# Kernel optimization log

Measured on AMD Instinct MI355X. Metric: run time of the kernel, lower is better.

The kernel has to match this reference:

```python
import jax, jax.numpy as jnp
import numpy as np


def rotate_half(x):
    x1, x2 = jnp.split(x, 2, axis=-1)
    return jnp.concatenate([-x2, x1], axis=-1)


def setup_inputs() -> dict:
    key = jax.random.key(0)
    ks = jax.random.split(key, 12)
    B, T, D, H, HD, MS = 1, 128, 4096, 32, 128, 8192
    s = 0.02  # weight init scale
    return {
        "x": jax.random.normal(ks[0], (B, T, D), jnp.float32),
        "wq_w": jax.random.normal(ks[1], (D, D), jnp.float32) * s,
        "wq_b": jax.random.normal(ks[2], (D,), jnp.float32) * s,
        "wk_w": jax.random.normal(ks[3], (D, D), jnp.float32) * s,
        "wk_b": jax.random.normal(ks[4], (D,), jnp.float32) * s,
        "wv_w": jax.random.normal(ks[5], (D, D), jnp.float32) * s,
        "wv_b": jax.random.normal(ks[6], (D,), jnp.float32) * s,
        "wo_w": jax.random.normal(ks[7], (D, D), jnp.float32) * s,
        "wo_b": jax.random.normal(ks[8], (D,), jnp.float32) * s,
        "k_cache": jax.random.normal(ks[9], (MS, H, HD), jnp.float32),
        "v_cache": jax.random.normal(ks[10], (MS, H, HD), jnp.float32),
        "pos": 4096,        # RoPE position scalar (as in source: single pos)
        "cache_pos": 4096,  # static write offset into the KV cache
    }


def reference(x, wq_w, wq_b, wk_w, wk_b, wv_w, wv_b, wo_w, wo_b,
              k_cache, v_cache, pos, cache_pos):
    B, T, D = x.shape
    H, HD = k_cache.shape[1], k_cache.shape[2]

    q = (x @ wq_w.T + wq_b).reshape(B, T, H, HD)
    k = (x @ wk_w.T + wk_b).reshape(B, T, H, HD)
    v = (x @ wv_w.T + wv_b).reshape(B, T, H, HD)

    # KV-cache append (B == 1, matching source's squeeze(0))
    k_cache = jax.lax.dynamic_update_slice(k_cache, k[0], (cache_pos, 0, 0))
    v_cache = jax.lax.dynamic_update_slice(v_cache, v[0], (cache_pos, 0, 0))
    S = cache_pos + T

    # inline RoPE at scalar position `pos` on q and the full live cache
    inv_freq = 1.0 / (10000.0 ** (jnp.arange(0, HD, 2, dtype=jnp.float32) / HD))
    ang = pos * inv_freq                      # [HD/2]
    sin = jnp.concatenate([jnp.sin(ang)] * 2) # [HD]
    cos = jnp.concatenate([jnp.cos(ang)] * 2) # [HD]

    kc = k_cache[:S][None]                    # [1, S, H, HD]
    vc = v_cache[:S][None]                    # [1, S, H, HD]
    q_rot = q * cos + rotate_half(q) * sin
    k_rot = kc * cos + rotate_half(kc) * sin

    scale = 1.0 / np.sqrt(HD).astype(np.float32)
    scores = jnp.einsum('bthd,bshd->bhts', q_rot, k_rot) * scale  # [B,H,T,S]
    attn = jax.nn.softmax(scores, axis=-1)
    out = jnp.einsum('bhts,bshd->bthd', attn, vc).reshape(B, T, D)
    return out @ wo_w.T + wo_b
```

## Files before the change

kernel.cpp:

```cpp
#include <hip/hip_runtime.h>

#define TQ     128
#define DIM    4096
#define NHEAD  32
#define HDIM   128
#define CPOS   4096
#define NCHUNK 8

typedef __attribute__((ext_vector_type(8))) short short8;
typedef __attribute__((ext_vector_type(4))) float f32x4;

__device__ __forceinline__ unsigned short f2bf(float f) {
    union { float f; unsigned int u; } v; v.f = f;
    unsigned int r = v.u + 0x7FFFu + ((v.u >> 16) & 1u);
    return (unsigned short)(r >> 16);
}

__global__ __launch_bounds__(256) void cvt_x_kernel(const float* __restrict__ x,
                                                    unsigned short* __restrict__ xbf) {
    int i = blockIdx.x * 256 + threadIdx.x;
    float4 v = ((const float4*)x)[i];
    union { unsigned short u[4]; uint2 w; } o;
    o.u[0] = f2bf(v.x); o.u[1] = f2bf(v.y); o.u[2] = f2bf(v.z); o.u[3] = f2bf(v.w);
    ((uint2*)xbf)[i] = o.w;
}

__global__ __launch_bounds__(256, 2) void qkv_gemm_kernel(
    const unsigned short* __restrict__ xbf,
    const float* __restrict__ wq, const float* __restrict__ wk, const float* __restrict__ wv,
    const float* __restrict__ bq, const float* __restrict__ bk, const float* __restrict__ bv,
    unsigned short* __restrict__ qbf, unsigned short* __restrict__ kbf,
    unsigned short* __restrict__ vbf)
{
    __shared__ unsigned short As[128 * 40];
    __shared__ unsigned short Bs[48 * 40];
    const int tid = threadIdx.x;
    const int w = tid >> 6, lane = tid & 63;
    const int q = lane >> 4, j = lane & 15;
    const int ncol0 = blockIdx.x * 48;

    f32x4 acc[2][3];
#pragma unroll
    for (int mi = 0; mi < 2; ++mi)
#pragma unroll
        for (int ni = 0; ni < 3; ++ni) acc[mi][ni] = (f32x4){0.f, 0.f, 0.f, 0.f};

    for (int it = 0; it < 128; ++it) {
        const int k0 = it * 32;
#pragma unroll
        for (int g = tid; g < 512; g += 256) {
            int row = g >> 2, col8 = (g & 3) * 8;
            uint4 d = *(const uint4*)(xbf + (size_t)row * DIM + k0 + col8);
            *(uint4*)(As + row * 40 + col8) = d;
        }
#pragma unroll
        for (int f = tid; f < 384; f += 256) {
            int row = f >> 3, col4 = (f & 7) * 4;
            int n = ncol0 + row;
            const float* wp = (n < 4096) ? wq : ((n < 8192) ? wk : wv);
            float4 d = *(const float4*)(wp + (size_t)(n & 4095) * DIM + k0 + col4);
            union { unsigned short u[4]; uint2 v; } o;
            o.u[0] = f2bf(d.x); o.u[1] = f2bf(d.y); o.u[2] = f2bf(d.z); o.u[3] = f2bf(d.w);
            *(uint2*)(Bs + row * 40 + col4) = o.v;
        }
        __syncthreads();
        short8 af[2], bfr[3];
#pragma unroll
        for (int mi = 0; mi < 2; ++mi)
            af[mi] = *(const short8*)(As + (w * 32 + mi * 16 + j) * 40 + q * 8);
#pragma unroll
        for (int ni = 0; ni < 3; ++ni)
            bfr[ni] = *(const short8*)(Bs + (ni * 16 + j) * 40 + q * 8);
#pragma unroll
        for (int mi = 0; mi < 2; ++mi)
#pragma unroll
            for (int ni = 0; ni < 3; ++ni)
                acc[mi][ni] = __builtin_amdgcn_mfma_f32_16x16x32_bf16(af[mi], bfr[ni], acc[mi][ni], 0, 0, 0);
        __syncthreads();
    }
#pragma unroll
    for (int ni = 0; ni < 3; ++ni) {
        int col = ncol0 + ni * 16 + j;
        int mat = col >> 12, nn = col & 4095;
        const float* bp = (mat == 0) ? bq : ((mat == 1) ? bk : bv);
        unsigned short* op = (mat == 0) ? qbf : ((mat == 1) ? kbf : vbf);
        float bias = bp[nn];
#pragma unroll
        for (int mi = 0; mi < 2; ++mi)
#pragma unroll
            for (int r = 0; r < 4; ++r) {
                int t = w * 32 + mi * 16 + q * 4 + r;
                op[(size_t)t * DIM + nn] = f2bf(acc[mi][ni][r] + bias);
            }
    }
}

__global__ __launch_bounds__(256, 2) void attn_kernel(
    const unsigned short* __restrict__ qbf, const unsigned short* __restrict__ kbf,
    const unsigned short* __restrict__ vbf,
    const float* __restrict__ kcache, const float* __restrict__ vcache,
    float* __restrict__ opart, float* __restrict__ ml)
{
    __shared__ unsigned short Ks[64 * 136];
    __shared__ unsigned short Vt[128 * 68];
    __shared__ unsigned short Ps[128 * 72];
    const int tid = threadIdx.x;
    const int w = tid >> 6, lane = tid & 63;
    const int q = lane >> 4, j = lane & 15;
    const int c = blockIdx.x, h = blockIdx.y;
    const int ntiles = (c == NCHUNK - 1) ? 10 : 8;
    const int s_base = c * 512;
    const float scale = 0.088388347648318447f;

    short8 qf[2][4];
#pragma unroll
    for (int mi = 0; mi < 2; ++mi) {
        int t = w * 32 + mi * 16 + j;
#pragma unroll
        for (int ks = 0; ks < 4; ++ks)
            qf[mi][ks] = *(const short8*)(qbf + (size_t)t * DIM + h * HDIM + ks * 32 + q * 8);
    }

    f32x4 oacc[2][8];
    float m_st[2][4], l_st[2][4];
#pragma unroll
    for (int mi = 0; mi < 2; ++mi) {
#pragma unroll
        for (int nh = 0; nh < 8; ++nh) oacc[mi][nh] = (f32x4){0.f, 0.f, 0.f, 0.f};
#pragma unroll
        for (int r = 0; r < 4; ++r) { m_st[mi][r] = -1e30f; l_st[mi][r] = 0.f; }
    }

    for (int tile = 0; tile < ntiles; ++tile) {
        const int s0 = s_base + tile * 64;
        const bool from_new = (s0 >= CPOS);
        if (!from_new) {
#pragma unroll
            for (int i = 0; i < 8; ++i) {
                int f = tid + i * 256;
                int row = f >> 5, col4 = (f & 31) * 4;
                float4 d = *(const float4*)(kcache + (size_t)(s0 + row) * DIM + h * HDIM + col4);
                union { unsigned short u[4]; uint2 v; } o;
                o.u[0] = f2bf(d.x); o.u[1] = f2bf(d.y); o.u[2] = f2bf(d.z); o.u[3] = f2bf(d.w);
                *(uint2*)(Ks + row * 136 + col4) = o.v;
            }
        } else {
            int sn = s0 - CPOS;
#pragma unroll
            for (int i = 0; i < 4; ++i) {
                int g = tid + i * 256;
                int row = g >> 4, col8 = (g & 15) * 8;
                uint4 d = *(const uint4*)(kbf + (size_t)(sn + row) * DIM + h * HDIM + col8);
                *(uint4*)(Ks + row * 136 + col8) = d;
            }
        }
        if (!from_new) {
#pragma unroll
            for (int i = 0; i < 2; ++i) {
                int ch = tid + i * 256;
                int s4 = ch >> 5, col4 = (ch & 31) * 4;
                const float* src = vcache + (size_t)(s0 + s4 * 4) * DIM + h * HDIM + col4;
                float4 r0 = *(const float4*)(src);
                float4 r1 = *(const float4*)(src + DIM);
                float4 r2 = *(const float4*)(src + 2 * DIM);
                float4 r3 = *(const float4*)(src + 3 * DIM);
#pragma unroll
                for (int i2 = 0; i2 < 4; ++i2) {
                    union { unsigned short u[4]; uint2 v; } o;
                    o.u[0] = f2bf((&r0.x)[i2]); o.u[1] = f2bf((&r1.x)[i2]);
                    o.u[2] = f2bf((&r2.x)[i2]); o.u[3] = f2bf((&r3.x)[i2]);
                    *(uint2*)(Vt + (col4 + i2) * 68 + s4 * 4) = o.v;
                }
            }
        } else {
            int sn = s0 - CPOS;
#pragma unroll
            for (int i = 0; i < 2; ++i) {
                int ch = tid + i * 256;
                int s4 = ch >> 5, col4 = (ch & 31) * 4;
                const unsigned short* src = vbf + (size_t)(sn + s4 * 4) * DIM + h * HDIM + col4;
                union { uint2 v; unsigned short u[4]; } a0, a1, a2, a3;
                a0.v = *(const uint2*)(src);
                a1.v = *(const uint2*)(src + DIM);
                a2.v = *(const uint2*)(src + 2 * DIM);
                a3.v = *(const uint2*)(src + 3 * DIM);
#pragma unroll
                for (int i2 = 0; i2 < 4; ++i2) {
                    union { unsigned short u[4]; uint2 v; } o;
                    o.u[0] = a0.u[i2]; o.u[1] = a1.u[i2]; o.u[2] = a2.u[i2]; o.u[3] = a3.u[i2];
                    *(uint2*)(Vt + (col4 + i2) * 68 + s4 * 4) = o.v;
                }
            }
        }
        __syncthreads();

        f32x4 sacc[2][4];
#pragma unroll
        for (int mi = 0; mi < 2; ++mi)
#pragma unroll
            for (int ni = 0; ni < 4; ++ni) sacc[mi][ni] = (f32x4){0.f, 0.f, 0.f, 0.f};
#pragma unroll
        for (int ks = 0; ks < 4; ++ks) {
            short8 kb[4];
#pragma unroll
            for (int ni = 0; ni < 4; ++ni)
                kb[ni] = *(const short8*)(Ks + (ni * 16 + j) * 136 + ks * 32 + q * 8);
#pragma unroll
            for (int mi = 0; mi < 2; ++mi)
#pragma unroll
                for (int ni = 0; ni < 4; ++ni)
                    sacc[mi][ni] = __builtin_amdgcn_mfma_f32_16x16x32_bf16(qf[mi][ks], kb[ni], sacc[mi][ni], 0, 0, 0);
        }

#pragma unroll
        for (int mi = 0; mi < 2; ++mi) {
            float alpha[4];
#pragma unroll
            for (int r = 0; r < 4; ++r) {
                float v = sacc[mi][0][r];
#pragma unroll
                for (int ni = 1; ni < 4; ++ni) v = fmaxf(v, sacc[mi][ni][r]);
#pragma unroll
                for (int mask = 1; mask < 16; mask <<= 1)
                    v = fmaxf(v, __shfl_xor(v, mask, 64));
                float mnew = fmaxf(m_st[mi][r], v * scale);
                alpha[r] = __expf(m_st[mi][r] - mnew);
                m_st[mi][r] = mnew;
            }
#pragma unroll
            for (int ni = 0; ni < 4; ++ni)
#pragma unroll
                for (int r = 0; r < 4; ++r)
                    sacc[mi][ni][r] = __expf(sacc[mi][ni][r] * scale - m_st[mi][r]);
#pragma unroll
            for (int r = 0; r < 4; ++r) {
                float s = sacc[mi][0][r] + sacc[mi][1][r] + sacc[mi][2][r] + sacc[mi][3][r];
#pragma unroll
                for (int mask = 1; mask < 16; mask <<= 1)
                    s += __shfl_xor(s, mask, 64);
                l_st[mi][r] = l_st[mi][r] * alpha[r] + s;
            }
#pragma unroll
            for (int ni = 0; ni < 4; ++ni)
#pragma unroll
                for (int r = 0; r < 4; ++r)
                    Ps[(w * 32 + mi * 16 + q * 4 + r) * 72 + ni * 16 + j] = f2bf(sacc[mi][ni][r]);
#pragma unroll
            for (int nh = 0; nh < 8; ++nh)
#pragma unroll
                for (int r = 0; r < 4; ++r)
                    oacc[mi][nh][r] *= alpha[r];
        }

#pragma unroll
        for (int ks2 = 0; ks2 < 2; ++ks2) {
            short8 pa[2];
#pragma unroll
            for (int mi = 0; mi < 2; ++mi)
                pa[mi] = *(const short8*)(Ps + (w * 32 + mi * 16 + j) * 72 + ks2 * 32 + q * 8);
#pragma unroll
            for (int nh = 0; nh < 8; ++nh) {
                const unsigned short* p = Vt + (nh * 16 + j) * 68 + ks2 * 32 + q * 8;
                uint2 lo = *(const uint2*)p, hi = *(const uint2*)(p + 4);
                union { unsigned int w4[4]; short8 s; } u;
                u.w4[0] = lo.x; u.w4[1] = lo.y; u.w4[2] = hi.x; u.w4[3] = hi.y;
#pragma unroll
                for (int mi = 0; mi < 2; ++mi)
                    oacc[mi][nh] = __builtin_amdgcn_mfma_f32_16x16x32_bf16(pa[mi], u.s, oacc[mi][nh], 0, 0, 0);
            }
        }
        __syncthreads();
    }

    float* op = opart + ((size_t)(h * NCHUNK + c) * TQ) * HDIM;
#pragma unroll
    for (int mi = 0; mi < 2; ++mi)
#pragma unroll
        for (int nh = 0; nh < 8; ++nh)
#pragma unroll
            for (int r = 0; r < 4; ++r) {
                int t = w * 32 + mi * 16 + q * 4 + r;
                op[(size_t)t * HDIM + nh * 16 + j] = oacc[mi][nh][r];
            }
    if (j == 0) {
        float* mlp = ml + (size_t)(h * NCHUNK + c) * TQ * 2;
#pragma unroll
        for (int mi = 0; mi < 2; ++mi)
#pragma unroll
            for (int r = 0; r < 4; ++r) {
                int t = w * 32 + mi * 16 + q * 4 + r;
                mlp[t * 2] = m_st[mi][r];
                mlp[t * 2 + 1] = l_st[mi][r];
            }
    }
}

__global__ __launch_bounds__(128) void combine_kernel(const float* __restrict__ opart,
                                                      const float* __restrict__ ml,
                                                      unsigned short* __restrict__ abf) {
    int t = blockIdx.x, h = blockIdx.y, hd = threadIdx.x;
    float mv[NCHUNK], lv[NCHUNK];
    float M = -1e30f;
#pragma unroll
    for (int c = 0; c < NCHUNK; ++c) {
        mv[c] = ml[(size_t)((h * NCHUNK + c) * TQ + t) * 2];
        lv[c] = ml[(size_t)((h * NCHUNK + c) * TQ + t) * 2 + 1];
        M = fmaxf(M, mv[c]);
    }
    float L = 0.f, acc = 0.f;
#pragma unroll
    for (int c = 0; c < NCHUNK; ++c) {
        float wgt = __expf(mv[c] - M);
        L += wgt * lv[c];
        acc += wgt * opart[((size_t)(h * NCHUNK + c) * TQ + t) * HDIM + hd];
    }
    abf[(size_t)t * DIM + h * HDIM + hd] = f2bf(acc / L);
}

__global__ __launch_bounds__(256, 2) void out_gemm_kernel(
    const unsigned short* __restrict__ abf, const float* __restrict__ wo,
    const float* __restrict__ bo, float* __restrict__ out)
{
    __shared__ unsigned short As[128 * 40];
    __shared__ unsigned short Bs[32 * 40];
    const int tid = threadIdx.x;
    const int w = tid >> 6, lane = tid & 63;
    const int q = lane >> 4, j = lane & 15;
    const int ncol0 = (blockIdx.x & 127) * 32;
    const int kc = blockIdx.x >> 7;

    f32x4 acc[2][2];
#pragma unroll
    for (int mi = 0; mi < 2; ++mi)
#pragma unroll
        for (int ni = 0; ni < 2; ++ni) acc[mi][ni] = (f32x4){0.f, 0.f, 0.f, 0.f};

    for (int it = 0; it < 64; ++it) {
        const int k0 = kc * 2048 + it * 32;
#pragma unroll
        for (int g = tid; g < 512; g += 256) {
            int row = g >> 2, col8 = (g & 3) * 8;
            uint4 d = *(const uint4*)(abf + (size_t)row * DIM + k0 + col8);
            *(uint4*)(As + row * 40 + col8) = d;
        }
        {
            int row = tid >> 3, col4 = (tid & 7) * 4;
            float4 d = *(const float4*)(wo + (size_t)(ncol0 + row) * DIM + k0 + col4);
            union { unsigned short u[4]; uint2 v; } o;
            o.u[0] = f2bf(d.x); o.u[1] = f2bf(d.y); o.u[2] = f2bf(d.z); o.u[3] = f2bf(d.w);
            *(uint2*)(Bs + row * 40 + col4) = o.v;
        }
        __syncthreads();
        short8 af[2], bfr[2];
#pragma unroll
        for (int mi = 0; mi < 2; ++mi)
            af[mi] = *(const short8*)(As + (w * 32 + mi * 16 + j) * 40 + q * 8);
#pragma unroll
        for (int ni = 0; ni < 2; ++ni)
            bfr[ni] = *(const short8*)(Bs + (ni * 16 + j) * 40 + q * 8);
#pragma unroll
        for (int mi = 0; mi < 2; ++mi)
#pragma unroll
            for (int ni = 0; ni < 2; ++ni)
                acc[mi][ni] = __builtin_amdgcn_mfma_f32_16x16x32_bf16(af[mi], bfr[ni], acc[mi][ni], 0, 0, 0);
        __syncthreads();
    }
#pragma unroll
    for (int ni = 0; ni < 2; ++ni) {
        int col = ncol0 + ni * 16 + j;
        float bias = (kc == 0) ? bo[col] : 0.f;
#pragma unroll
        for (int mi = 0; mi < 2; ++mi)
#pragma unroll
            for (int r = 0; r < 4; ++r) {
                int t = w * 32 + mi * 16 + q * 4 + r;
                atomicAdd(out + (size_t)t * DIM + col, acc[mi][ni][r] + bias);
            }
    }
}

extern "C" void kernel_launch(void* const* d_in, const int* in_sizes, int n_in,
                              void* d_out, int out_size, void* d_ws, size_t ws_size,
                              hipStream_t stream) {
    const float* x      = (const float*)d_in[0];
    const float* wq     = (const float*)d_in[1];
    const float* bq     = (const float*)d_in[2];
    const float* wk     = (const float*)d_in[3];
    const float* bk     = (const float*)d_in[4];
    const float* wv     = (const float*)d_in[5];
    const float* bv     = (const float*)d_in[6];
    const float* wo     = (const float*)d_in[7];
    const float* bo     = (const float*)d_in[8];
    const float* kcache = (const float*)d_in[9];
    const float* vcache = (const float*)d_in[10];
    float* out = (float*)d_out;

    char* ws = (char*)d_ws;
    unsigned short* xbf = (unsigned short*)(ws);
    unsigned short* qbf = (unsigned short*)(ws + (1u << 20));
    unsigned short* kbf = (unsigned short*)(ws + 2u * (1u << 20));
    unsigned short* vbf = (unsigned short*)(ws + 3u * (1u << 20));
    unsigned short* abf = (unsigned short*)(ws + 4u * (1u << 20));
    float* opart = (float*)(ws + 5u * (1u << 20));
    float* mlbuf = (float*)(ws + 21u * (1u << 20));

    hipLaunchKernelGGL(cvt_x_kernel, dim3(512), dim3(256), 0, stream, x, xbf);
    hipLaunchKernelGGL(qkv_gemm_kernel, dim3(256), dim3(256), 0, stream,
                       xbf, wq, wk, wv, bq, bk, bv, qbf, kbf, vbf);
    hipLaunchKernelGGL(attn_kernel, dim3(NCHUNK, NHEAD), dim3(256), 0, stream,
                       qbf, kbf, vbf, kcache, vcache, opart, mlbuf);
    hipLaunchKernelGGL(combine_kernel, dim3(TQ, NHEAD), dim3(128), 0, stream,
                       opart, mlbuf, abf);
    hipMemsetAsync(d_out, 0, (size_t)out_size * sizeof(float), stream);
    hipLaunchKernelGGL(out_gemm_kernel, dim3(256), dim3(256), 0, stream, abf, wo, bo, out);
}
```

Baseline: 683.6 us.

## Split-K QKV and output GEMMs with reductions, more attention chunks, register prefetch

The QKV GEMM is split along K across a second grid dimension, writes fp32 partials, and a new reduce kernel adds bias and converts to bf16. The output GEMM drops atomics and memset in favour of split-K partials plus a reduce kernel. Attention uses more sequence chunks, with a dedicated chunk for the new tokens. The GEMMs now use 64-wide K tiles with register double-buffered global loads and higher launch-bounds occupancy. Together these add parallelism on a 256-CU device at the cost of extra partial-buffer traffic and two more launches.

```diff
diff --git a/kernel.cpp b/kernel.cpp
--- a/kernel.cpp
+++ b/kernel.cpp
@@ -5,7 +5,6 @@
 #define NHEAD  32
 #define HDIM   128
 #define CPOS   4096
-#define NCHUNK 8
 
 typedef __attribute__((ext_vector_type(8))) short short8;
 typedef __attribute__((ext_vector_type(4))) float f32x4;
@@ -25,19 +24,21 @@
     ((uint2*)xbf)[i] = o.w;
 }
 
-__global__ __launch_bounds__(256, 2) void qkv_gemm_kernel(
+__global__ __launch_bounds__(256, 4) void qkv_gemm_kernel(
     const unsigned short* __restrict__ xbf,
     const float* __restrict__ wq, const float* __restrict__ wk, const float* __restrict__ wv,
-    const float* __restrict__ bq, const float* __restrict__ bk, const float* __restrict__ bv,
-    unsigned short* __restrict__ qbf, unsigned short* __restrict__ kbf,
-    unsigned short* __restrict__ vbf)
+    float* __restrict__ part)
 {
-    __shared__ unsigned short As[128 * 40];
-    __shared__ unsigned short Bs[48 * 40];
+    __shared__ unsigned short As[128 * 72];
+    __shared__ unsigned short Bs[48 * 72];
     const int tid = threadIdx.x;
     const int w = tid >> 6, lane = tid & 63;
     const int q = lane >> 4, j = lane & 15;
     const int ncol0 = blockIdx.x * 48;
+    const int kc = blockIdx.y, KS = gridDim.y;
+    const int kchunk = DIM / KS;
+    const int iters = kchunk / 64;
+    const int kbase = kc * kchunk;
 
     f32x4 acc[2][3];
 #pragma unroll
@@ -45,61 +46,114 @@
 #pragma unroll
         for (int ni = 0; ni < 3; ++ni) acc[mi][ni] = (f32x4){0.f, 0.f, 0.f, 0.f};
 
-    for (int it = 0; it < 128; ++it) {
-        const int k0 = it * 32;
-#pragma unroll
-        for (int g = tid; g < 512; g += 256) {
-            int row = g >> 2, col8 = (g & 3) * 8;
-            uint4 d = *(const uint4*)(xbf + (size_t)row * DIM + k0 + col8);
-            *(uint4*)(As + row * 40 + col8) = d;
-        }
-#pragma unroll
-        for (int f = tid; f < 384; f += 256) {
-            int row = f >> 3, col4 = (f & 7) * 4;
-            int n = ncol0 + row;
+    uint4 aReg[4];
+    float4 bReg[3];
+    {
+        const int k0 = kbase;
+#pragma unroll
+        for (int i = 0; i < 4; ++i) {
+            int flat = i * 256 + tid;
+            aReg[i] = *(const uint4*)(xbf + (size_t)(flat >> 3) * DIM + k0 + (flat & 7) * 8);
+        }
+#pragma unroll
+        for (int i = 0; i < 3; ++i) {
+            int flat = i * 256 + tid;
+            int n = ncol0 + (flat >> 4);
             const float* wp = (n < 4096) ? wq : ((n < 8192) ? wk : wv);
-            float4 d = *(const float4*)(wp + (size_t)(n & 4095) * DIM + k0 + col4);
+            bReg[i] = *(const float4*)(wp + (size_t)(n & 4095) * DIM + k0 + (flat & 15) * 4);
+        }
+    }
+
+    for (int it = 0; it < iters; ++it) {
+        if (it > 0) __syncthreads();
+#pragma unroll
+        for (int i = 0; i < 4; ++i) {
+            int flat = i * 256 + tid;
+            *(uint4*)(As + (flat >> 3) * 72 + (flat & 7) * 8) = aReg[i];
+        }
+#pragma unroll
+        for (int i = 0; i < 3; ++i) {
+            int flat = i * 256 + tid;
             union { unsigned short u[4]; uint2 v; } o;
-            o.u[0] = f2bf(d.x); o.u[1] = f2bf(d.y); o.u[2] = f2bf(d.z); o.u[3] = f2bf(d.w);
-            *(uint2*)(Bs + row * 40 + col4) = o.v;
+            o.u[0] = f2bf(bReg[i].x); o.u[1] = f2bf(bReg[i].y);
+            o.u[2] = f2bf(bReg[i].z); o.u[3] = f2bf(bReg[i].w);
+            *(uint2*)(Bs + (flat >> 4) * 72 + (flat & 15) * 4) = o.v;
         }
         __syncthreads();
-        short8 af[2], bfr[3];
-#pragma unroll
-        for (int mi = 0; mi < 2; ++mi)
-            af[mi] = *(const short8*)(As + (w * 32 + mi * 16 + j) * 40 + q * 8);
-#pragma unroll
-        for (int ni = 0; ni < 3; ++ni)
-            bfr[ni] = *(const short8*)(Bs + (ni * 16 + j) * 40 + q * 8);
-#pragma unroll
-        for (int mi = 0; mi < 2; ++mi)
+        if (it + 1 < iters) {
+            const int k0 = kbase + (it + 1) * 64;
+#pragma unroll
+            for (int i = 0; i < 4; ++i) {
+                int flat = i * 256 + tid;
+                aReg[i] = *(const uint4*)(xbf + (size_t)(flat >> 3) * DIM + k0 + (flat & 7) * 8);
+            }
+#pragma unroll
+            for (int i = 0; i < 3; ++i) {
+                int flat = i * 256 + tid;
+                int n = ncol0 + (flat >> 4);
+                const float* wp = (n < 4096) ? wq : ((n < 8192) ? wk : wv);
+                bReg[i] = *(const float4*)(wp + (size_t)(n & 4095) * DIM + k0 + (flat & 15) * 4);
+            }
+        }
+#pragma unroll
+        for (int ks = 0; ks < 2; ++ks) {
+            short8 af[2], bfr[3];
+#pragma unroll
+            for (int mi = 0; mi < 2; ++mi)
+                af[mi] = *(const short8*)(As + (w * 32 + mi * 16 + j) * 72 + ks * 32 + q * 8);
 #pragma unroll
             for (int ni = 0; ni < 3; ++ni)
-                acc[mi][ni] = __builtin_amdgcn_mfma_f32_16x16x32_bf16(af[mi], bfr[ni], acc[mi][ni], 0, 0, 0);
-        __syncthreads();
-    }
+                bfr[ni] = *(const short8*)(Bs + (ni * 16 + j) * 72 + ks * 32 + q * 8);
+#pragma unroll
+            for (int mi = 0; mi < 2; ++mi)
+#pragma unroll
+                for (int ni = 0; ni < 3; ++ni)
+                    acc[mi][ni] = __builtin_amdgcn_mfma_f32_16x16x32_bf16(af[mi], bfr[ni], acc[mi][ni], 0, 0, 0);
+        }
+    }
+    float* pp = part + (size_t)kc * (TQ * 12288);
 #pragma unroll
     for (int ni = 0; ni < 3; ++ni) {
         int col = ncol0 + ni * 16 + j;
-        int mat = col >> 12, nn = col & 4095;
-        const float* bp = (mat == 0) ? bq : ((mat == 1) ? bk : bv);
-        unsigned short* op = (mat == 0) ? qbf : ((mat == 1) ? kbf : vbf);
-        float bias = bp[nn];
 #pragma unroll
         for (int mi = 0; mi < 2; ++mi)
 #pragma unroll
             for (int r = 0; r < 4; ++r) {
                 int t = w * 32 + mi * 16 + q * 4 + r;
-                op[(size_t)t * DIM + nn] = f2bf(acc[mi][ni][r] + bias);
-            }
-    }
+                pp[(size_t)t * 12288 + col] = acc[mi][ni][r];
+            }
+    }
+}
+
+__global__ __launch_bounds__(256) void qkv_reduce_kernel(
+    const float* __restrict__ part,
+    const float* __restrict__ bq, const float* __restrict__ bk, const float* __restrict__ bv,
+    unsigned short* __restrict__ qbf, unsigned short* __restrict__ kbf,
+    unsigned short* __restrict__ vbf, int KS)
+{
+    int idx4 = blockIdx.x * 256 + threadIdx.x;
+    size_t idx = (size_t)idx4 * 4;
+    int t = (int)(idx / 12288), n = (int)(idx % 12288);
+    float4 s = *(const float4*)(part + idx);
+    for (int kc = 1; kc < KS; ++kc) {
+        float4 p = *(const float4*)(part + (size_t)kc * (TQ * 12288) + idx);
+        s.x += p.x; s.y += p.y; s.z += p.z; s.w += p.w;
+    }
+    int mat = n >> 12, nn = n & 4095;
+    const float* bp = (mat == 0) ? bq : ((mat == 1) ? bk : bv);
+    unsigned short* op = (mat == 0) ? qbf : ((mat == 1) ? kbf : vbf);
+    float4 b = *(const float4*)(bp + nn);
+    union { unsigned short u[4]; uint2 v; } o;
+    o.u[0] = f2bf(s.x + b.x); o.u[1] = f2bf(s.y + b.y);
+    o.u[2] = f2bf(s.z + b.z); o.u[3] = f2bf(s.w + b.w);
+    *(uint2*)(op + (size_t)t * 4096 + nn) = o.v;
 }
 
 __global__ __launch_bounds__(256, 2) void attn_kernel(
     const unsigned short* __restrict__ qbf, const unsigned short* __restrict__ kbf,
     const unsigned short* __restrict__ vbf,
     const float* __restrict__ kcache, const float* __restrict__ vcache,
-    float* __restrict__ opart, float* __restrict__ ml)
+    float* __restrict__ opart, float* __restrict__ ml, int c_tiles)
 {
     __shared__ unsigned short Ks[64 * 136];
     __shared__ unsigned short Vt[128 * 68];
@@ -108,8 +162,10 @@
     const int w = tid >> 6, lane = tid & 63;
     const int q = lane >> 4, j = lane & 15;
     const int c = blockIdx.x, h = blockIdx.y;
-    const int ntiles = (c == NCHUNK - 1) ? 10 : 8;
-    const int s_base = c * 512;
+    const int nchunk = gridDim.x;
+    const bool is_new = (c == nchunk - 1);
+    const int ntiles = is_new ? 2 : c_tiles;
+    const int s_base = c * c_tiles * 64;
     const float scale = 0.088388347648318447f;
 
     short8 qf[2][4];
@@ -132,9 +188,8 @@
     }
 
     for (int tile = 0; tile < ntiles; ++tile) {
-        const int s0 = s_base + tile * 64;
-        const bool from_new = (s0 >= CPOS);
-        if (!from_new) {
+        if (!is_new) {
+            const int s0 = s_base + tile * 64;
 #pragma unroll
             for (int i = 0; i < 8; ++i) {
                 int f = tid + i * 256;
@@ -145,7 +200,7 @@
                 *(uint2*)(Ks + row * 136 + col4) = o.v;
             }
         } else {
-            int sn = s0 - CPOS;
+            int sn = tile * 64;
 #pragma unroll
             for (int i = 0; i < 4; ++i) {
                 int g = tid + i * 256;
@@ -154,7 +209,8 @@
                 *(uint4*)(Ks + row * 136 + col8) = d;
             }
         }
-        if (!from_new) {
+        if (!is_new) {
+            const int s0 = s_base + tile * 64;
 #pragma unroll
             for (int i = 0; i < 2; ++i) {
                 int ch = tid + i * 256;
@@ -173,7 +229,7 @@
                 }
             }
         } else {
-            int sn = s0 - CPOS;
+            int sn = tile * 64;
 #pragma unroll
             for (int i = 0; i < 2; ++i) {
                 int ch = tid + i * 256;
@@ -272,7 +328,7 @@
         __syncthreads();
     }
 
-    float* op = opart + ((size_t)(h * NCHUNK + c) * TQ) * HDIM;
+    float* op = opart + ((size_t)(h * nchunk + c) * TQ) * HDIM;
 #pragma unroll
     for (int mi = 0; mi < 2; ++mi)
 #pragma unroll
@@ -283,7 +339,7 @@
                 op[(size_t)t * HDIM + nh * 16 + j] = oacc[mi][nh][r];
             }
     if (j == 0) {
-        float* mlp = ml + (size_t)(h * NCHUNK + c) * TQ * 2;
+        float* mlp = ml + (size_t)(h * nchunk + c) * TQ * 2;
 #pragma unroll
         for (int mi = 0; mi < 2; ++mi)
 #pragma unroll
@@ -297,37 +353,37 @@
 
 __global__ __launch_bounds__(128) void combine_kernel(const float* __restrict__ opart,
                                                       const float* __restrict__ ml,
-                                                      unsigned short* __restrict__ abf) {
+                                                      unsigned short* __restrict__ abf,
+                                                      int nchunk) {
     int t = blockIdx.x, h = blockIdx.y, hd = threadIdx.x;
-    float mv[NCHUNK], lv[NCHUNK];
     float M = -1e30f;
-#pragma unroll
-    for (int c = 0; c < NCHUNK; ++c) {
-        mv[c] = ml[(size_t)((h * NCHUNK + c) * TQ + t) * 2];
-        lv[c] = ml[(size_t)((h * NCHUNK + c) * TQ + t) * 2 + 1];
-        M = fmaxf(M, mv[c]);
-    }
+    for (int c = 0; c < nchunk; ++c)
+        M = fmaxf(M, ml[(size_t)((h * nchunk + c) * TQ + t) * 2]);
     float L = 0.f, acc = 0.f;
-#pragma unroll
-    for (int c = 0; c < NCHUNK; ++c) {
-        float wgt = __expf(mv[c] - M);
-        L += wgt * lv[c];
-        acc += wgt * opart[((size_t)(h * NCHUNK + c) * TQ + t) * HDIM + hd];
+    for (int c = 0; c < nchunk; ++c) {
+        float m = ml[(size_t)((h * nchunk + c) * TQ + t) * 2];
+        float l = ml[(size_t)((h * nchunk + c) * TQ + t) * 2 + 1];
+        float wgt = __expf(m - M);
+        L += wgt * l;
+        acc += wgt * opart[((size_t)(h * nchunk + c) * TQ + t) * HDIM + hd];
     }
     abf[(size_t)t * DIM + h * HDIM + hd] = f2bf(acc / L);
 }
 
-__global__ __launch_bounds__(256, 2) void out_gemm_kernel(
+__global__ __launch_bounds__(256, 4) void out_gemm_kernel(
     const unsigned short* __restrict__ abf, const float* __restrict__ wo,
-    const float* __restrict__ bo, float* __restrict__ out)
+    float* __restrict__ part)
 {
-    __shared__ unsigned short As[128 * 40];
-    __shared__ unsigned short Bs[32 * 40];
+    __shared__ unsigned short As[128 * 72];
+    __shared__ unsigned short Bs[32 * 72];
     const int tid = threadIdx.x;
     const int w = tid >> 6, lane = tid & 63;
     const int q = lane >> 4, j = lane & 15;
-    const int ncol0 = (blockIdx.x & 127) * 32;
-    const int kc = blockIdx.x >> 7;
+    const int ncol0 = blockIdx.x * 32;
+    const int kc = blockIdx.y, KO = gridDim.y;
+    const int kchunk = DIM / KO;
+    const int iters = kchunk / 64;
+    const int kbase = kc * kchunk;
 
     f32x4 acc[2][2];
 #pragma unroll
@@ -335,48 +391,96 @@
 #pragma unroll
         for (int ni = 0; ni < 2; ++ni) acc[mi][ni] = (f32x4){0.f, 0.f, 0.f, 0.f};
 
-    for (int it = 0; it < 64; ++it) {
-        const int k0 = kc * 2048 + it * 32;
-#pragma unroll
-        for (int g = tid; g < 512; g += 256) {
-            int row = g >> 2, col8 = (g & 3) * 8;
-            uint4 d = *(const uint4*)(abf + (size_t)row * DIM + k0 + col8);
-            *(uint4*)(As + row * 40 + col8) = d;
-        }
-        {
-            int row = tid >> 3, col4 = (tid & 7) * 4;
-            float4 d = *(const float4*)(wo + (size_t)(ncol0 + row) * DIM + k0 + col4);
+    uint4 aReg[4];
+    float4 bReg[2];
+    {
+        const int k0 = kbase;
+#pragma unroll
+        for (int i = 0; i < 4; ++i) {
+            int flat = i * 256 + tid;
+            aReg[i] = *(const uint4*)(abf + (size_t)(flat >> 3) * DIM + k0 + (flat & 7) * 8);
+        }
+#pragma unroll
+        for (int i = 0; i < 2; ++i) {
+            int flat = i * 256 + tid;
+            bReg[i] = *(const float4*)(wo + (size_t)(ncol0 + (flat >> 4)) * DIM + k0 + (flat & 15) * 4);
+        }
+    }
+
+    for (int it = 0; it < iters; ++it) {
+        if (it > 0) __syncthreads();
+#pragma unroll
+        for (int i = 0; i < 4; ++i) {
+            int flat = i * 256 + tid;
+            *(uint4*)(As + (flat >> 3) * 72 + (flat & 7) * 8) = aReg[i];
+        }
+#pragma unroll
+        for (int i = 0; i < 2; ++i) {
+            int flat = i * 256 + tid;
             union { unsigned short u[4]; uint2 v; } o;
-            o.u[0] = f2bf(d.x); o.u[1] = f2bf(d.y); o.u[2] = f2bf(d.z); o.u[3] = f2bf(d.w);
-            *(uint2*)(Bs + row * 40 + col4) = o.v;
+            o.u[0] = f2bf(bReg[i].x); o.u[1] = f2bf(bReg[i].y);
+            o.u[2] = f2bf(bReg[i].z); o.u[3] = f2bf(bReg[i].w);
+            *(uint2*)(Bs + (flat >> 4) * 72 + (flat & 15) * 4) = o.v;
         }
         __syncthreads();
-        short8 af[2], bfr[2];
-#pragma unroll
-        for (int mi = 0; mi < 2; ++mi)
-            af[mi] = *(const short8*)(As + (w * 32 + mi * 16 + j) * 40 + q * 8);
-#pragma unroll
-        for (int ni = 0; ni < 2; ++ni)
-            bfr[ni] = *(const short8*)(Bs + (ni * 16 + j) * 40 + q * 8);
-#pragma unroll
-        for (int mi = 0; mi < 2; ++mi)
+        if (it + 1 < iters) {
+            const int k0 = kbase + (it + 1) * 64;
+#pragma unroll
+            for (int i = 0; i < 4; ++i) {
+                int flat = i * 256 + tid;
+                aReg[i] = *(const uint4*)(abf + (size_t)(flat >> 3) * DIM + k0 + (flat & 7) * 8);
+            }
+#pragma unroll
+            for (int i = 0; i < 2; ++i) {
+                int flat = i * 256 + tid;
+                bReg[i] = *(const float4*)(wo + (size_t)(ncol0 + (flat >> 4)) * DIM + k0 + (flat & 15) * 4);
+            }
+        }
+#pragma unroll
+        for (int ks = 0; ks < 2; ++ks) {
+            short8 af[2], bfr[2];
+#pragma unroll
+            for (int mi = 0; mi < 2; ++mi)
+                af[mi] = *(const short8*)(As + (w * 32 + mi * 16 + j) * 72 + ks * 32 + q * 8);
 #pragma unroll
             for (int ni = 0; ni < 2; ++ni)
-                acc[mi][ni] = __builtin_amdgcn_mfma_f32_16x16x32_bf16(af[mi], bfr[ni], acc[mi][ni], 0, 0, 0);
-        __syncthreads();
-    }
+                bfr[ni] = *(const short8*)(Bs + (ni * 16 + j) * 72 + ks * 32 + q * 8);
+#pragma unroll
+            for (int mi = 0; mi < 2; ++mi)
+#pragma unroll
+                for (int ni = 0; ni < 2; ++ni)
+                    acc[mi][ni] = __builtin_amdgcn_mfma_f32_16x16x32_bf16(af[mi], bfr[ni], acc[mi][ni], 0, 0, 0);
+        }
+    }
+    float* pp = part + (size_t)kc * (TQ * DIM);
 #pragma unroll
     for (int ni = 0; ni < 2; ++ni) {
         int col = ncol0 + ni * 16 + j;
-        float bias = (kc == 0) ? bo[col] : 0.f;
 #pragma unroll
         for (int mi = 0; mi < 2; ++mi)
 #pragma unroll
             for (int r = 0; r < 4; ++r) {
                 int t = w * 32 + mi * 16 + q * 4 + r;
-                atomicAdd(out + (size_t)t * DIM + col, acc[mi][ni][r] + bias);
-            }
-    }
+                pp[(size_t)t * DIM + col] = acc[mi][ni][r];
+            }
+    }
+}
+
+__global__ __launch_bounds__(256) void out_reduce_kernel(
+    const float* __restrict__ part, const float* __restrict__ bo,
+    float* __restrict__ out, int KO)
+{
+    int idx4 = blockIdx.x * 256 + threadIdx.x;
+    size_t idx = (size_t)idx4 * 4;
+    int col = (int)(idx % DIM);
+    float4 s = *(const float4*)(part + idx);
+    for (int kc = 1; kc < KO; ++kc) {
+        float4 p = *(const float4*)(part + (size_t)kc * (TQ * DIM) + idx);
+        s.x += p.x; s.y += p.y; s.z += p.z; s.w += p.w;
+    }
+    float4 b = *(const float4*)(bo + col);
+    s.x += b.x; s.y += b.y; s.z += b.z; s.w += b.w;
+    *(float4*)(out + idx) = s;
 }
 
 extern "C" void kernel_launch(void* const* d_in, const int* in_sizes, int n_in,
@@ -395,22 +499,37 @@
     const float* vcache = (const float*)d_in[10];
     float* out = (float*)d_out;
 
+    const size_t MB = 1u << 20;
     char* ws = (char*)d_ws;
     unsigned short* xbf = (unsigned short*)(ws);
-    unsigned short* qbf = (unsigned short*)(ws + (1u << 20));
-    unsigned short* kbf = (unsigned short*)(ws + 2u * (1u << 20));
-    unsigned short* vbf = (unsigned short*)(ws + 3u * (1u << 20));
-    unsigned short* abf = (unsigned short*)(ws + 4u * (1u << 20));
-    float* opart = (float*)(ws + 5u * (1u << 20));
-    float* mlbuf = (float*)(ws + 21u * (1u << 20));
+    unsigned short* qbf = (unsigned short*)(ws + 1 * MB);
+    unsigned short* kbf = (unsigned short*)(ws + 2 * MB);
+    unsigned short* vbf = (unsigned short*)(ws + 3 * MB);
+    unsigned short* abf = (unsigned short*)(ws + 4 * MB);
+    char* pool = ws + 5 * MB;
+
+    int KS, CCH, KO;
+    if (ws_size >= 43 * MB) { KS = 4; CCH = 16; KO = 8; }
+    else                    { KS = 2; CCH = 8;  KO = 4; }
+    const int c_tiles = (CPOS / CCH) / 64;
+    const int nchunk = CCH + 1;
+
+    float* part_qkv = (float*)pool;
+    float* opart    = (float*)pool;
+    float* mlbuf    = (float*)(pool + (size_t)nchunk * NHEAD * TQ * HDIM * 4);
+    float* part_out = (float*)pool;
 
     hipLaunchKernelGGL(cvt_x_kernel, dim3(512), dim3(256), 0, stream, x, xbf);
-    hipLaunchKernelGGL(qkv_gemm_kernel, dim3(256), dim3(256), 0, stream,
-                       xbf, wq, wk, wv, bq, bk, bv, qbf, kbf, vbf);
-    hipLaunchKernelGGL(attn_kernel, dim3(NCHUNK, NHEAD), dim3(256), 0, stream,
-                       qbf, kbf, vbf, kcache, vcache, opart, mlbuf);
+    hipLaunchKernelGGL(qkv_gemm_kernel, dim3(256, KS), dim3(256), 0, stream,
+                       xbf, wq, wk, wv, part_qkv);
+    hipLaunchKernelGGL(qkv_reduce_kernel, dim3(1536), dim3(256), 0, stream,
+                       part_qkv, bq, bk, bv, qbf, kbf, vbf, KS);
+    hipLaunchKernelGGL(attn_kernel, dim3(nchunk, NHEAD), dim3(256), 0, stream,
+                       qbf, kbf, vbf, kcache, vcache, opart, mlbuf, c_tiles);
     hipLaunchKernelGGL(combine_kernel, dim3(TQ, NHEAD), dim3(128), 0, stream,
-                       opart, mlbuf, abf);
-    hipMemsetAsync(d_out, 0, (size_t)out_size * sizeof(float), stream);
-    hipLaunchKernelGGL(out_gemm_kernel, dim3(256), dim3(256), 0, stream, abf, wo, bo, out);
-}
+                       opart, mlbuf, abf, nchunk);
+    hipLaunchKernelGGL(out_gemm_kernel, dim3(128, KO), dim3(256), 0, stream,
+                       abf, wo, part_out);
+    hipLaunchKernelGGL(out_reduce_kernel, dim3(512), dim3(256), 0, stream,
+                       part_out, bo, out, KO);
+}
```

New measurement: 565.5 us. -17.3%, faster.
